# Performance work log

Hardware: AMD Instinct MI355X
Metric: run time of the kernel (lower is better)

The kernel has to match this reference:

```python
import jax, jax.numpy as jnp
import numpy as np

N = 100000          # total nodes in batch of junction trees
H = 256             # hidden_size
K = 8               # MAX_NUM_NEIGHBORS (padded neighbor slots)


def setup_inputs() -> dict:
    key = jax.random.key(0)
    k1, k2, k3, k4, k5, k6, k7 = jax.random.split(key, 7)
    scale = 1.0 / np.sqrt(H)
    inputs = {
        "prev_layer_output": jax.random.normal(k1, (N, H), dtype=jnp.float32),
        "W_U": jax.random.uniform(k2, (H, H), jnp.float32, -scale, scale),
        "W_V": jax.random.uniform(k3, (H, H), jnp.float32, -scale, scale),
        "W_A": jax.random.uniform(k4, (H, H), jnp.float32, -scale, scale),
        "W_B": jax.random.uniform(k5, (H, H), jnp.float32, -scale, scale),
        "parent_idxs": jnp.arange(N, dtype=jnp.int32),
        "child_idxs": jax.random.randint(k6, (N, K), 0, N, dtype=jnp.int32),
        "child_mask": jax.random.randint(k7, (N, K), 0, 2, dtype=jnp.int32).astype(jnp.bool_),
    }
    return inputs


def reference(prev_layer_output, W_U, W_V, W_A, W_B, parent_idxs, child_idxs, child_mask):
    # Gather parent hidden states: [E, H]
    ph = prev_layer_output[parent_idxs]
    # Gather child hidden states, zeroing padded slots (faithful to the
    # zero-vector padding in the original): [E, K, H]
    ch = jnp.where(child_mask[..., None], prev_layer_output[child_idxs], 0.0)

    # Edge gates: eta = sigmoid(A(parent)[:,None] + B(child)).
    # Padded slots still contribute sigmoid(A(parent)) — matches original.
    A_h = jnp.einsum('eh,ih->ei', ph, W_A)            # [E, H]
    B_h = jnp.einsum('ekh,ih->eki', ch, W_B)          # [E, K, H]
    eta = jax.nn.sigmoid(A_h[:, None, :] + B_h)       # [E, K, H]

    # Graph convolution: relu(U(parent) + sum_k (eta + V(child)))
    # NOTE: original ADDS eta to V_h (despite the 'mul' variable name).
    U_h = jnp.einsum('eh,ih->ei', ph, W_U)            # [E, H]
    V_h = jnp.einsum('ekh,ih->eki', ch, W_V)          # [E, K, H]
    new_h = jax.nn.relu(U_h + jnp.sum(eta + V_h, axis=1))  # [E, H]

    # Scatter into the current layer output (rows not updated stay zero).
    current = jnp.zeros_like(prev_layer_output).at[parent_idxs].set(new_h)
    return current
```

## Files before the change

kernel.cpp:

```cpp
#include <hip/hip_runtime.h>

#define HH 256
#define KK 8

typedef __attribute__((ext_vector_type(8))) short s16x8;
typedef __attribute__((ext_vector_type(4))) float f32x4;

__device__ __forceinline__ float bf2f(unsigned short u){ unsigned x=((unsigned)u)<<16; return __builtin_bit_cast(float,x); }
__device__ __forceinline__ unsigned f2bf(float f){ unsigned x=__builtin_bit_cast(unsigned,f); return (x+0x7fffu+((x>>16)&1u))>>16; }
__device__ __forceinline__ float sigmoidf(float x){ return __builtin_amdgcn_rcpf(1.0f + __expf(-x)); }

__global__ void cvt_w(const float* __restrict__ wa, const float* __restrict__ wu,
                      const float* __restrict__ wv, const float* __restrict__ wbm,
                      unsigned short* __restrict__ dst){
  const int w = blockIdx.y;
  const float* src = (w==0)? wa : (w==1)? wu : (w==2)? wv : wbm;
  const int i = blockIdx.x*256 + threadIdx.x;
  const float4* s = reinterpret_cast<const float4*>(src);
  float4 a = s[i*2], b = s[i*2+1];
  uint4 o;
  o.x = f2bf(a.x) | (f2bf(a.y)<<16);
  o.y = f2bf(a.z) | (f2bf(a.w)<<16);
  o.z = f2bf(b.x) | (f2bf(b.y)<<16);
  o.w = f2bf(b.z) | (f2bf(b.w)<<16);
  reinterpret_cast<uint4*>(dst + (size_t)w*65536)[i] = o;
}

__global__ __launch_bounds__(512, 2)
void gemm_all(const float* __restrict__ prev,
              const unsigned short* __restrict__ wb,
              unsigned short* __restrict__ px,
              int n)
{
  __shared__ char smem[81920];
  char* bs = smem + 65536;
  const int tid = threadIdx.x;
  const int m0  = blockIdx.x * 128;
  const int lane = tid & 63, wid = tid >> 6;
  const int wr = wid >> 1, wc = wid & 1;
  const int lm = lane & 15, kc = lane >> 4;
  const int srow0 = tid >> 3, sch = tid & 7;
  const char* wbc = reinterpret_cast<const char*>(wb);

  uint4 P0a, P0b, P1a, P1b;
  {
    const char* g0 = wbc + srow0*512 + sch*16;
    P0a = *reinterpret_cast<const uint4*>(g0);
    P0b = *reinterpret_cast<const uint4*>(g0 + 32768);
    const char* g1 = wbc + 128 + srow0*512 + sch*16;
    P1a = *reinterpret_cast<const uint4*>(g1);
    P1b = *reinterpret_cast<const uint4*>(g1 + 32768);
  }

  #pragma unroll
  for (int it=0; it<8; ++it){
    const int c = it*512 + tid;
    const int row = c>>5, kch = c&31;
    const int gm = m0 + row;
    uint4 o = {0u,0u,0u,0u};
    if (gm < n){
      const float4* sp = reinterpret_cast<const float4*>(prev + (size_t)gm*HH + kch*8);
      float4 f0 = sp[0], f1 = sp[1];
      o.x=f2bf(f0.x)|(f2bf(f0.y)<<16);
      o.y=f2bf(f0.z)|(f2bf(f0.w)<<16);
      o.z=f2bf(f1.x)|(f2bf(f1.y)<<16);
      o.w=f2bf(f1.z)|(f2bf(f1.w)<<16);
    }
    *reinterpret_cast<uint4*>(smem + row*512 + ((kch*16) ^ ((row&7)<<4))) = o;
  }
  __syncthreads();

  f32x4 acc[2][4];

  #define STEP(q_, Pa, Pb)                                                        \
  {                                                                               \
    __builtin_amdgcn_s_barrier();                    \
    { const int swb = (srow0&7)<<4;                                               \
      *reinterpret_cast<uint4*>(bs + srow0*128 + ((sch*16) ^ swb)) = Pa;          \
      *reinterpret_cast<uint4*>(bs + (srow0+64)*128 + ((sch*16) ^ swb)) = Pb; }   \
    asm volatile("s_waitcnt lgkmcnt(0)" ::: "memory");                            \
    __builtin_amdgcn_s_barrier();                              \
    __builtin_amdgcn_sched_barrier(0);                                            \
    if ((q_) + 2 < 32){                                                           \
      const int p2_ = (q_) + 2;                                                   \
      const char* gb_ = wbc + (p2_>>2)*65536 + (p2_&3)*128 + srow0*512 + sch*16;  \
      Pa = *reinterpret_cast<const uint4*>(gb_);                                  \
      Pb = *reinterpret_cast<const uint4*>(gb_ + 32768);                          \
    }                                                                             \
    const int ks_ = (q_)&3, g_ = (q_)>>2;                                         \
    if (ks_==0){                                                                  \
      _Pragma("unroll")                                                           \
      for (int i_=0;i_<2;++i_){ _Pragma("unroll")                                 \
        for (int j_=0;j_<4;++j_) acc[i_][j_]=(f32x4){0.f,0.f,0.f,0.f}; }          \
    }                                                                             \
    __builtin_amdgcn_s_setprio(1);                                                \
    _Pragma("unroll")                                                             \
    for (int kk_=0; kk_<2; ++kk_){                                                \
      s16x8 a0_, a1_;                                                             \
      { const int row_ = wr*32 + lm;                                              \
        a0_ = *reinterpret_cast<const s16x8*>(smem + row_*512                     \
              + ((ks_*128 + kk_*64 + kc*16) ^ ((row_&7)<<4))); }                  \
      { const int row_ = wr*32 + 16 + lm;                                         \
        a1_ = *reinterpret_cast<const s16x8*>(smem + row_*512                     \
              + ((ks_*128 + kk_*64 + kc*16) ^ ((row_&7)<<4))); }                  \
      _Pragma("unroll")                                                           \
      for (int j_=0;j_<4;++j_){                                                   \
        const int brow_ = wc*64 + j_*16 + lm;                                     \
        s16x8 b_ = *reinterpret_cast<const s16x8*>(bs + brow_*128                 \
              + ((kk_*64 + kc*16) ^ ((brow_&7)<<4)));                             \
        acc[0][j_] = __builtin_amdgcn_mfma_f32_16x16x32_bf16(a0_, b_, acc[0][j_], 0,0,0); \
        acc[1][j_] = __builtin_amdgcn_mfma_f32_16x16x32_bf16(a1_, b_, acc[1][j_], 0,0,0); \
      }                                                                           \
    }                                                                             \
    __builtin_amdgcn_s_setprio(0);                                                \
    if (ks_==3){                                                                  \
      _Pragma("unroll")                                                           \
      for (int i_=0;i_<2;++i_){ _Pragma("unroll")                                 \
        for (int r_=0;r_<4;++r_){                                                 \
          const int gm_ = m0 + wr*32 + i_*16 + kc*4 + r_;                         \
          if (gm_ < n){                                                           \
            unsigned short* dp_ = px + (size_t)gm_*1024 + g_*128 + wc*64 + lm;    \
            _Pragma("unroll")                                                     \
            for (int j_=0;j_<4;++j_) dp_[j_*16] = (unsigned short)f2bf(acc[i_][j_][r_]); \
          } } }                                                                   \
    }                                                                             \
  }

  #pragma unroll
  for (int qq=0; qq<16; ++qq){
    STEP(qq*2,   P0a, P0b)
    STEP(qq*2+1, P1a, P1b)
  }
  #undef STEP
}

__global__ __launch_bounds__(256)
void epilogue(const unsigned short* __restrict__ px,
              const int* __restrict__ parent,
              const int* __restrict__ child,
              const int* __restrict__ mask,
              float* __restrict__ out,
              int n)
{
  const int e = blockIdx.x*4 + (threadIdx.x>>6);
  if (e >= n) return;
  const int c4 = (threadIdx.x & 63) * 4;
  const int p  = parent[e];

  const unsigned short* rp = px + (size_t)p*1024 + c4;
  uint2 av = *reinterpret_cast<const uint2*>(rp);
  uint2 uv = *reinterpret_cast<const uint2*>(rp + 256);
  const unsigned short* ap = reinterpret_cast<const unsigned short*>(&av);
  const unsigned short* up = reinterpret_cast<const unsigned short*>(&uv);

  float A[4], o[4], eta[4];
  #pragma unroll
  for (int j=0;j<4;++j){ A[j]=bf2f(ap[j]); o[j]=bf2f(up[j]); eta[j]=0.f; }

  int nm = 0;
  #pragma unroll
  for (int k=0;k<KK;++k){
    if (mask[(size_t)e*KK + k]){
      const unsigned short* rc = px + (size_t)child[(size_t)e*KK + k]*1024 + c4;
      uint2 pv = *reinterpret_cast<const uint2*>(rc + 512);
      uint2 pb = *reinterpret_cast<const uint2*>(rc + 768);
      const unsigned short* vp = reinterpret_cast<const unsigned short*>(&pv);
      const unsigned short* bp = reinterpret_cast<const unsigned short*>(&pb);
      #pragma unroll
      for (int j=0;j<4;++j){
        o[j]   += bf2f(vp[j]);
        eta[j] += sigmoidf(A[j] + bf2f(bp[j]));
      }
    } else ++nm;
  }

  const float fnm = (float)nm;
  float4 r;
  {
    float v0 = o[0] + eta[0] + fnm*sigmoidf(A[0]);
    float v1 = o[1] + eta[1] + fnm*sigmoidf(A[1]);
    float v2 = o[2] + eta[2] + fnm*sigmoidf(A[2]);
    float v3 = o[3] + eta[3] + fnm*sigmoidf(A[3]);
    r.x = v0>0.f?v0:0.f; r.y = v1>0.f?v1:0.f;
    r.z = v2>0.f?v2:0.f; r.w = v3>0.f?v3:0.f;
  }
  *reinterpret_cast<float4*>(out + (size_t)p*HH + c4) = r;
}

extern "C" void kernel_launch(void* const* d_in, const int* in_sizes, int n_in,
                              void* d_out, int out_size, void* d_ws, size_t ws_size,
                              hipStream_t stream)
{
  const float* prev = (const float*)d_in[0];
  const float* W_U  = (const float*)d_in[1];
  const float* W_V  = (const float*)d_in[2];
  const float* W_A  = (const float*)d_in[3];
  const float* W_B  = (const float*)d_in[4];
  const int* parent = (const int*)d_in[5];
  const int* child  = (const int*)d_in[6];
  const int* mask   = (const int*)d_in[7];
  float* out = (float*)d_out;

  const int n_nodes = in_sizes[5];

  unsigned short* wb = (unsigned short*)d_ws;
  unsigned short* px = wb + 4*65536;

  dim3 gc(32, 4);
  cvt_w<<<gc, 256, 0, stream>>>(W_A, W_U, W_V, W_B, wb);

  gemm_all<<<(n_nodes + 127)/128, 512, 0, stream>>>(prev, wb, px, n_nodes);

  epilogue<<<(n_nodes + 3)/4, 256, 0, stream>>>(px, parent, child, mask, out, n_nodes);
}
```

Before: 227.4 us.

## Retile weight GEMM to 64x64 warp tiles with full-width double-buffered B stages

Restructures the batched weight GEMM so each stage loads a 256-column by 64-k slab of the bf16 weights into a double-buffered LDS region, instead of 128-column slabs. Warps are rearranged to a 2x4 grid, each computing a 64x64 output tile with 4x4 MFMA accumulators, which raises A/B register reuse per LDS read. The pipeline drops from 32 to 16 stages and from two barriers per stage to one. LDS use grows to 128 KB and accumulator registers double, which may limit occupancy to one block per CU despite launch_bounds(512,2).

```diff
diff --git a/kernel.cpp b/kernel.cpp
--- a/kernel.cpp
+++ b/kernel.cpp
@@ -32,24 +32,26 @@
               unsigned short* __restrict__ px,
               int n)
 {
-  __shared__ char smem[81920];
-  char* bs = smem + 65536;
+  __shared__ char smem[131072];
+  char* const bsb = smem + 65536;
   const int tid = threadIdx.x;
   const int m0  = blockIdx.x * 128;
   const int lane = tid & 63, wid = tid >> 6;
-  const int wr = wid >> 1, wc = wid & 1;
+  const int wr = wid >> 2, wc = wid & 3;
   const int lm = lane & 15, kc = lane >> 4;
-  const int srow0 = tid >> 3, sch = tid & 7;
+
+  const int colL = tid >> 1;
+  const int ch0  = (tid & 1) * 64;
+  const int cswz = (colL & 7) << 4;
   const char* wbc = reinterpret_cast<const char*>(wb);
 
-  uint4 P0a, P0b, P1a, P1b;
+  uint4 pre0, pre1, pre2, pre3;
   {
-    const char* g0 = wbc + srow0*512 + sch*16;
-    P0a = *reinterpret_cast<const uint4*>(g0);
-    P0b = *reinterpret_cast<const uint4*>(g0 + 32768);
-    const char* g1 = wbc + 128 + srow0*512 + sch*16;
-    P1a = *reinterpret_cast<const uint4*>(g1);
-    P1b = *reinterpret_cast<const uint4*>(g1 + 32768);
+    const char* g = wbc + (size_t)colL*512 + ch0;
+    pre0 = *reinterpret_cast<const uint4*>(g);
+    pre1 = *reinterpret_cast<const uint4*>(g + 16);
+    pre2 = *reinterpret_cast<const uint4*>(g + 32);
+    pre3 = *reinterpret_cast<const uint4*>(g + 48);
   }
 
   #pragma unroll
@@ -68,70 +70,68 @@
     }
     *reinterpret_cast<uint4*>(smem + row*512 + ((kch*16) ^ ((row&7)<<4))) = o;
   }
-  __syncthreads();
-
-  f32x4 acc[2][4];
-
-  #define STEP(q_, Pa, Pb)                                                        \
-  {                                                                               \
-    __builtin_amdgcn_s_barrier();                    \
-    { const int swb = (srow0&7)<<4;                                               \
-      *reinterpret_cast<uint4*>(bs + srow0*128 + ((sch*16) ^ swb)) = Pa;          \
-      *reinterpret_cast<uint4*>(bs + (srow0+64)*128 + ((sch*16) ^ swb)) = Pb; }   \
-    asm volatile("s_waitcnt lgkmcnt(0)" ::: "memory");                            \
-    __builtin_amdgcn_s_barrier();                              \
-    __builtin_amdgcn_sched_barrier(0);                                            \
-    if ((q_) + 2 < 32){                                                           \
-      const int p2_ = (q_) + 2;                                                   \
-      const char* gb_ = wbc + (p2_>>2)*65536 + (p2_&3)*128 + srow0*512 + sch*16;  \
-      Pa = *reinterpret_cast<const uint4*>(gb_);                                  \
-      Pb = *reinterpret_cast<const uint4*>(gb_ + 32768);                          \
-    }                                                                             \
-    const int ks_ = (q_)&3, g_ = (q_)>>2;                                         \
-    if (ks_==0){                                                                  \
-      _Pragma("unroll")                                                           \
-      for (int i_=0;i_<2;++i_){ _Pragma("unroll")                                 \
-        for (int j_=0;j_<4;++j_) acc[i_][j_]=(f32x4){0.f,0.f,0.f,0.f}; }          \
-    }                                                                             \
-    __builtin_amdgcn_s_setprio(1);                                                \
-    _Pragma("unroll")                                                             \
-    for (int kk_=0; kk_<2; ++kk_){                                                \
-      s16x8 a0_, a1_;                                                             \
-      { const int row_ = wr*32 + lm;                                              \
-        a0_ = *reinterpret_cast<const s16x8*>(smem + row_*512                     \
-              + ((ks_*128 + kk_*64 + kc*16) ^ ((row_&7)<<4))); }                  \
-      { const int row_ = wr*32 + 16 + lm;                                         \
-        a1_ = *reinterpret_cast<const s16x8*>(smem + row_*512                     \
-              + ((ks_*128 + kk_*64 + kc*16) ^ ((row_&7)<<4))); }                  \
-      _Pragma("unroll")                                                           \
-      for (int j_=0;j_<4;++j_){                                                   \
-        const int brow_ = wc*64 + j_*16 + lm;                                     \
-        s16x8 b_ = *reinterpret_cast<const s16x8*>(bs + brow_*128                 \
-              + ((kk_*64 + kc*16) ^ ((brow_&7)<<4)));                             \
-        acc[0][j_] = __builtin_amdgcn_mfma_f32_16x16x32_bf16(a0_, b_, acc[0][j_], 0,0,0); \
-        acc[1][j_] = __builtin_amdgcn_mfma_f32_16x16x32_bf16(a1_, b_, acc[1][j_], 0,0,0); \
-      }                                                                           \
-    }                                                                             \
-    __builtin_amdgcn_s_setprio(0);                                                \
-    if (ks_==3){                                                                  \
-      _Pragma("unroll")                                                           \
-      for (int i_=0;i_<2;++i_){ _Pragma("unroll")                                 \
-        for (int r_=0;r_<4;++r_){                                                 \
-          const int gm_ = m0 + wr*32 + i_*16 + kc*4 + r_;                         \
-          if (gm_ < n){                                                           \
-            unsigned short* dp_ = px + (size_t)gm_*1024 + g_*128 + wc*64 + lm;    \
-            _Pragma("unroll")                                                     \
-            for (int j_=0;j_<4;++j_) dp_[j_*16] = (unsigned short)f2bf(acc[i_][j_][r_]); \
-          } } }                                                                   \
-    }                                                                             \
-  }
-
-  #pragma unroll
-  for (int qq=0; qq<16; ++qq){
-    STEP(qq*2,   P0a, P0b)
-    STEP(qq*2+1, P1a, P1b)
-  }
-  #undef STEP
+
+  f32x4 acc[4][4];
+
+  for (int q=0; q<16; ++q){
+    const int cg = q>>2, ks = q&3;
+    {
+      char* bb = bsb + (q&1)*32768;
+      *reinterpret_cast<uint4*>(bb + colL*128 + ((ch0      ) ^ cswz)) = pre0;
+      *reinterpret_cast<uint4*>(bb + colL*128 + ((ch0 + 16 ) ^ cswz)) = pre1;
+      *reinterpret_cast<uint4*>(bb + colL*128 + ((ch0 + 32 ) ^ cswz)) = pre2;
+      *reinterpret_cast<uint4*>(bb + colL*128 + ((ch0 + 48 ) ^ cswz)) = pre3;
+    }
+    __syncthreads();
+    if (q < 15){
+      const int p1 = q+1;
+      const char* g = wbc + (size_t)(((p1>>2)*256) + colL)*512 + (p1&3)*128 + ch0;
+      pre0 = *reinterpret_cast<const uint4*>(g);
+      pre1 = *reinterpret_cast<const uint4*>(g + 16);
+      pre2 = *reinterpret_cast<const uint4*>(g + 32);
+      pre3 = *reinterpret_cast<const uint4*>(g + 48);
+    }
+    if (ks == 0){
+      #pragma unroll
+      for (int i=0;i<4;++i)
+        #pragma unroll
+        for (int j=0;j<4;++j) acc[i][j]=(f32x4){0.f,0.f,0.f,0.f};
+    }
+    const char* rb = bsb + (q&1)*32768;
+    #pragma unroll
+    for (int kk=0; kk<2; ++kk){
+      s16x8 a[4];
+      #pragma unroll
+      for (int i=0;i<4;++i){
+        const int row = wr*64 + i*16 + lm;
+        a[i] = *reinterpret_cast<const s16x8*>(smem + row*512
+                 + ((ks*128 + kk*64 + kc*16) ^ ((row&7)<<4)));
+      }
+      #pragma unroll
+      for (int j=0;j<4;++j){
+        const int brow = wc*64 + j*16 + lm;
+        s16x8 b = *reinterpret_cast<const s16x8*>(rb + brow*128
+                 + ((kk*64 + kc*16) ^ ((brow&7)<<4)));
+        #pragma unroll
+        for (int i=0;i<4;++i)
+          acc[i][j] = __builtin_amdgcn_mfma_f32_16x16x32_bf16(a[i], b, acc[i][j], 0, 0, 0);
+      }
+    }
+    if (ks == 3){
+      #pragma unroll
+      for (int i=0;i<4;++i){
+        #pragma unroll
+        for (int r=0;r<4;++r){
+          const int gm = m0 + wr*64 + i*16 + kc*4 + r;
+          if (gm < n){
+            unsigned short* dp = px + (size_t)gm*1024 + cg*256 + wc*64 + lm;
+            #pragma unroll
+            for (int j=0;j<4;++j) dp[j*16] = (unsigned short)f2bf(acc[i][j][r]);
+          }
+        }
+      }
+    }
+  }
 }
 
 __global__ __launch_bounds__(256)
```

After: 248.2 us. 1.09x slower.
